# Performance work log

Hardware: AMD Instinct MI355X
Metric: run time of the kernel (lower is better)

The kernel has to match this reference:

```python
import jax, jax.numpy as jnp
import numpy as np

# Config mirroring My_MLP(mlp_layers=2, isize=512, k=30, non_linearity='relu',
#                        mlp_act='relu', offset_list=[2048]*4)
SIZES = [2048, 2048, 2048, 2048]   # per-client subgraph sizes (offset_list)
N = sum(SIZES)                      # 8192 total nodes
D = 512                             # isize
K = 30 + 1                          # module uses self.k + 1


def setup_inputs() -> dict:
    key = jax.random.key(0)
    k1, k2, k3 = jax.random.split(key, 3)
    features = jax.random.normal(k1, (N, D), dtype=jnp.float32)
    # Diag layer weights: a learned diagonal (vector) per layer, init near 1.
    w0 = 1.0 + 0.1 * jax.random.normal(k2, (D,), dtype=jnp.float32)
    w1 = 1.0 + 0.1 * jax.random.normal(k3, (D,), dtype=jnp.float32)
    return {"features": features, "w0": w0, "w1": w1}


def reference(features, w0, w1):
    # internal_forward: Diag -> relu -> Diag (no act after last layer)
    h = jax.nn.relu(features * w0) * w1                 # [N, D]
    # F.normalize(dim=1, p=2)
    emb = h * jax.lax.rsqrt(jnp.sum(h * h, axis=1, keepdims=True) + 1e-24)
    sim = jnp.matmul(emb, emb.T)                        # [N, N]

    # cross_subgraph_topk: per row, keep top-(k+1) similarities among columns
    # belonging to a DIFFERENT client subgraph; zero everything else.
    seg = jnp.asarray(np.repeat(np.arange(len(SIZES)), SIZES))   # [N] int
    same = seg[:, None] == seg[None, :]                           # [N, N] bool
    masked = jnp.where(same, -jnp.inf, sim)
    vals, inds = jax.lax.top_k(masked, K)                         # [N, K]
    rows = jnp.arange(N)[:, None]
    out = jnp.zeros_like(sim).at[rows, inds].set(vals)

    # apply_non_linearity('relu', i)
    return jax.nn.relu(out)
```

## Files before the change

kernel.cpp:

```cpp
#include <hip/hip_runtime.h>
#include <hip/hip_bf16.h>
#include <hip/hip_fp16.h>
#include <math.h>

typedef unsigned short u16;
typedef unsigned int u32;
typedef unsigned long long u64;
typedef __attribute__((ext_vector_type(8))) short bf16x8;
typedef __attribute__((ext_vector_type(4))) float f32x4;

#define N_NODES 8192
#define DIM 512
#define KSEL 31
#define BANDCAP 128
#define SEG_SIZE 2048
#define NVALID 6144
#define BAND_ULP 8

__device__ __forceinline__ u32 f16key(u32 h) {
  return (h & 0x8000u) ? (0xFFFFu & ~h) : (h | 0x8000u);
}
__device__ __forceinline__ u32 packkeys(u32 w) {
  return f16key(w & 0xFFFFu) | (f16key(w >> 16) << 16);
}
__device__ __forceinline__ float keyval(u32 k) {
  const u16 raw = (k & 0x8000u) ? (u16)(k ^ 0x8000u) : (u16)(~k & 0xFFFFu);
  __half_raw hr; hr.x = raw;
  return __half2float(__half(hr));
}

#define GLD_LDS16(g, l)                                        \
  __builtin_amdgcn_global_load_lds(                            \
      (const __attribute__((address_space(1))) void*)(g),      \
      (__attribute__((address_space(3))) void*)(l), 16, 0, 0)

__global__ __launch_bounds__(256) void prep_kernel(
    const float* __restrict__ feat, const float* __restrict__ w0,
    const float* __restrict__ w1, u16* __restrict__ embh,
    float* __restrict__ embf, u32* __restrict__ kmax32) {
#pragma clang fp contract(off)
  const int row = blockIdx.x;
  const int t = threadIdx.x;
  __shared__ float hs[DIM];
  __shared__ float partial[32];
  __shared__ float rinv_sh;

  const float2 x = *reinterpret_cast<const float2*>(feat + (size_t)row * DIM + t * 2);
  const float2 a = *reinterpret_cast<const float2*>(w0 + t * 2);
  const float2 b = *reinterpret_cast<const float2*>(w1 + t * 2);
  const float h0 = fmaxf(x.x * a.x, 0.0f) * b.x;
  const float h1 = fmaxf(x.y * a.y, 0.0f) * b.y;
  hs[t * 2] = h0;
  hs[t * 2 + 1] = h1;
  if (t == 0) kmax32[row] = 0u;
  __syncthreads();

  if (t < 32) {
    const int base = (t >> 3) * 128 + (t & 7);
    float v = hs[base];
    float acc = v * v;
    for (int i = 1; i < 16; ++i) {
      v = hs[base + 8 * i];
      const float vv = v * v;
      acc = acc + vv;
    }
    partial[t] = acc;
  }
  __syncthreads();
  if (t == 0) {
    float B[4];
    for (int blk = 0; blk < 4; ++blk) {
      const float* p = &partial[blk * 8];
      B[blk] = ((p[0] + p[1]) + (p[2] + p[3])) + ((p[4] + p[5]) + (p[6] + p[7]));
    }
    const float s = (B[0] + B[1]) + (B[2] + B[3]);
    const float sp = s + 1e-24f;
    const float qf = (float)sqrt((double)sp);
    rinv_sh = (float)(1.0 / (double)qf);
  }
  __syncthreads();
  const float rinv = rinv_sh;
  const float e0 = h0 * rinv;
  const float e1 = h1 * rinv;
  *reinterpret_cast<float2*>(embf + (size_t)row * DIM + t * 2) = make_float2(e0, e1);
  __hip_bfloat162 bb;
  bb.x = __float2bfloat16(e0);
  bb.y = __float2bfloat16(e1);
  *reinterpret_cast<__hip_bfloat162*>(embh + (size_t)row * DIM + t * 2) = bb;
}

__global__ __launch_bounds__(256) void gemm_kernel(const u16* __restrict__ embh,
                                                   __half* __restrict__ simh,
                                                   u32* __restrict__ kmax32) {
  const int tid = threadIdx.x;
  const int lane = tid & 63;
  const int wave = tid >> 6;
  const int wm = wave >> 1;
  const int wn = wave & 1;
  const int rowTile = blockIdx.y;
  const int segTileBase = (rowTile >> 4) << 4;
  const int cT = blockIdx.x;
  const int colTile = cT < segTileBase ? cT : cT + 16;
  if (colTile <= rowTile) return;
  const int row0 = rowTile * 128;
  const int col0 = colTile * 128;

  __shared__ u16 As[128][64];
  __shared__ u16 Bs[128][64];
  f32x4 acc[4][4] = {};

  for (int k0 = 0; k0 < DIM; k0 += 64) {
#pragma unroll
    for (int i = 0; i < 4; ++i) {
      const int flat = i * 256 + tid;
      const int r = flat >> 3;
      const int c = (flat & 7) * 8;
      GLD_LDS16(embh + (size_t)(row0 + r) * DIM + k0 + c, &As[r][c]);
      GLD_LDS16(embh + (size_t)(col0 + r) * DIM + k0 + c, &Bs[r][c]);
    }
    __syncthreads();
#pragma unroll
    for (int kk = 0; kk < 2; ++kk) {
      bf16x8 afr[4], bfr[4];
      const int koff = kk * 32 + (lane >> 4) * 8;
      const int rsel = lane & 15;
#pragma unroll
      for (int m = 0; m < 4; ++m)
        afr[m] = *reinterpret_cast<const bf16x8*>(&As[wm * 64 + m * 16 + rsel][koff]);
#pragma unroll
      for (int n = 0; n < 4; ++n)
        bfr[n] = *reinterpret_cast<const bf16x8*>(&Bs[wn * 64 + n * 16 + rsel][koff]);
#pragma unroll
      for (int m = 0; m < 4; ++m)
#pragma unroll
        for (int n = 0; n < 4; ++n)
          acc[m][n] = __builtin_amdgcn_mfma_f32_16x16x32_bf16(afr[m], bfr[n],
                                                              acc[m][n], 0, 0, 0);
    }
    __syncthreads();
  }

#pragma unroll
  for (int m = 0; m < 4; ++m)
#pragma unroll
    for (int n = 0; n < 4; ++n)
#pragma unroll
      for (int j = 0; j < 4; ++j) {
        const int r = row0 + wm * 64 + m * 16 + (lane >> 4) * 4 + j;
        const int pcol = cT * 128 + wn * 64 + n * 16 + (lane & 15);
        simh[(size_t)r * NVALID + pcol] = __float2half(acc[m][n][j]);
      }
  {
    const int segBaseC = (col0 >> 11) << 11;
    const int radj = (row0 < segBaseC) ? 0 : -SEG_SIZE;
#pragma unroll
    for (int m = 0; m < 4; ++m)
#pragma unroll
      for (int n = 0; n < 4; ++n) {
        const int c = col0 + wn * 64 + n * 16 + (lane & 15);
        const int rbase = row0 + wm * 64 + m * 16 + (lane >> 4) * 4;
        const __half h0 = __float2half(acc[m][n][0]);
        const __half h1 = __float2half(acc[m][n][1]);
        const __half h2 = __float2half(acc[m][n][2]);
        const __half h3 = __float2half(acc[m][n][3]);
        uint2 pkd;
        pkd.x = (u32)__half_as_ushort(h0) | ((u32)__half_as_ushort(h1) << 16);
        pkd.y = (u32)__half_as_ushort(h2) | ((u32)__half_as_ushort(h3) << 16);
        *reinterpret_cast<uint2*>(&simh[(size_t)c * NVALID + radj + rbase]) = pkd;
      }
  }
#pragma unroll
  for (int m = 0; m < 4; ++m) {
#pragma unroll
    for (int j = 0; j < 4; ++j) {
      float vmax = fmaxf(fmaxf(acc[m][0][j], acc[m][1][j]),
                         fmaxf(acc[m][2][j], acc[m][3][j]));
#pragma unroll
      for (int off = 1; off < 16; off <<= 1)
        vmax = fmaxf(vmax, __shfl_xor(vmax, off, 64));
      if ((lane & 15) == 0) {
        const int r = row0 + wm * 64 + m * 16 + (lane >> 4) * 4 + j;
        const u32 b = __float_as_uint(vmax);
        const u32 kk = (b & 0x80000000u) ? ~b : (b | 0x80000000u);
        atomicMax(&kmax32[r], kk);
      }
    }
  }
#pragma unroll
  for (int n = 0; n < 4; ++n) {
    float cmax = acc[0][n][0];
#pragma unroll
    for (int m = 0; m < 4; ++m)
#pragma unroll
      for (int j = 0; j < 4; ++j) cmax = fmaxf(cmax, acc[m][n][j]);
    cmax = fmaxf(cmax, __shfl_xor(cmax, 16, 64));
    cmax = fmaxf(cmax, __shfl_xor(cmax, 32, 64));
    if ((lane >> 4) == 0) {
      const int c = col0 + wn * 64 + n * 16 + (lane & 15);
      const u32 b = __float_as_uint(cmax);
      const u32 kk = (b & 0x80000000u) ? ~b : (b | 0x80000000u);
      atomicMax(&kmax32[c], kk);
    }
  }
}

__global__ __launch_bounds__(256) void select_kernel(
    const __half* __restrict__ simh, const float* __restrict__ embf,
    const u32* __restrict__ kmax32, int2* __restrict__ compact) {
  const int row = blockIdx.x;
  const int t = threadIdx.x;
  const int lane = t & 63;
  const int wave = t >> 6;

  __shared__ u32 hist[257];
  __shared__ int bcol[BANDCAP];
  __shared__ u32 bkey[BANDCAP];
  __shared__ float bex[BANDCAP];
  __shared__ int outidx_s[KSEL];
  __shared__ float outval_s[KSEL];
  __shared__ int cnts[2];
  __shared__ u32 sh_lo, sh_hi, sh_need;
  __shared__ int sh_state;

  const int segBase = (row >> 11) << 11;

  u32 pk[12];
  {
    const uint4* src = reinterpret_cast<const uint4*>(simh + (size_t)row * NVALID);
    const uint4 a = src[t], b = src[256 + t], c = src[512 + t];
    pk[0] = packkeys(a.x); pk[1] = packkeys(a.y);
    pk[2] = packkeys(a.z); pk[3] = packkeys(a.w);
    pk[4] = packkeys(b.x); pk[5] = packkeys(b.y);
    pk[6] = packkeys(b.z); pk[7] = packkeys(b.w);
    pk[8] = packkeys(c.x); pk[9] = packkeys(c.y);
    pk[10] = packkeys(c.z); pk[11] = packkeys(c.w);
  }
#define KEY(v) ((pk[(v) >> 1] >> (((v) & 1) * 16)) & 0xFFFFu)
#define COL(v) ((((((v) >> 3) * 256) + t) << 3) + ((v) & 7))

  if (t < KSEL) { outidx_s[t] = segBase; outval_s[t] = 0.0f; }
  if (t == 0) { cnts[0] = 0; cnts[1] = 0; }

  u32 kmax16;
  {
    const u32 kk = kmax32[row];
    const u32 fb = (kk & 0x80000000u) ? (kk ^ 0x80000000u) : ~kk;
    const __half h = __float2half(__uint_as_float(fb));
    kmax16 = f16key((u32)__half_as_ushort(h));
  }

  u32 base = (kmax16 > 4095u) ? kmax16 - 4095u : 0u;
  u32 winTop = kmax16;
  u32 shift = 4;
  u32 need = KSEL;
  for (int guard = 0; guard < 4; ++guard) {
    hist[t] = 0;
    if (t == 0) hist[256] = 0;
    __syncthreads();
#pragma unroll
    for (int v = 0; v < 24; ++v) {
      const u32 k = KEY(v);
      if (k >= base && k <= winTop) atomicAdd(&hist[(k - base) >> shift], 1u);
    }
    __syncthreads();
    if (wave == 0) {
      const int x = lane * 4;
      const u32 b0 = hist[x], b1 = hist[x + 1];
      const u32 b2 = hist[x + 2], b3 = hist[x + 3];
      const u32 tot = b0 + b1 + b2 + b3;
      u32 inc = tot;
#pragma unroll
      for (int off = 1; off < 64; off <<= 1) {
        const u32 vv = (u32)__shfl_down((int)inc, off, 64);
        if (lane + off < 64) inc += vv;
      }
      const u32 exc = inc - tot;
      const u32 g3 = exc, g2 = g3 + b3, g1 = g2 + b2, g0 = g1 + b1;
      int sel = -1;
      u32 gsel = 0;
      if (g3 < need && g3 + b3 >= need) { sel = x + 3; gsel = g3; }
      else if (g2 < need && g2 + b2 >= need) { sel = x + 2; gsel = g2; }
      else if (g1 < need && g1 + b1 >= need) { sel = x + 1; gsel = g1; }
      else if (g0 < need && g0 + b0 >= need) { sel = x;     gsel = g0; }
      const u64 bal = __ballot(sel >= 0);
      if (lane == 0 && bal == 0) sh_state = 0;
      if (bal != 0) {
        const int srcl = (int)(__ffsll((unsigned long long)bal) - 1);
        sel  = __shfl(sel, srcl, 64);
        gsel = (u32)__shfl((int)gsel, srcl, 64);
        if (lane == 0) {
          const u32 blo = base + ((u32)sel << shift);
          const u32 bhi = min(blo + (1u << shift) - 1u, winTop);
          sh_lo = blo; sh_hi = bhi; sh_need = need - gsel;
          sh_state = (shift > 4) ? 1 : 2;
        }
      }
    }
    __syncthreads();
    const int st = sh_state;
    if (st == 2) break;
    if (st == 1) {
      base = sh_lo; winTop = sh_hi; shift = 4; need = sh_need;
    } else {
      base = 0u; winTop = kmax16; shift = 8; need = KSEL;
    }
    __syncthreads();
  }
  const u32 binlo = sh_lo, binhi = sh_hi;
  const u32 hiK = binhi + BAND_ULP;
  const u32 loK = (binlo >= BAND_ULP) ? binlo - BAND_ULP : 0u;

#pragma unroll
  for (int v = 0; v < 24; ++v) {
    const u32 k = KEY(v);
    if (k > hiK) {
      const int slot = atomicAdd(&cnts[1], 1);
      const int i = COL(v);
      if (slot < KSEL) {
        outidx_s[slot] = (i < segBase) ? i : i + SEG_SIZE;
        outval_s[slot] = fmaxf(keyval(k), 0.0f);
      }
    } else if (k >= loK) {
      const int slot = atomicAdd(&cnts[0], 1);
      const int i = COL(v);
      if (slot < BANDCAP) {
        bcol[slot] = (i < segBase) ? i : i + SEG_SIZE;
        bkey[slot] = k;
      }
    }
  }
  __syncthreads();
  const int nH = min(cnts[1], KSEL);
  const int slots = KSEL - nH;
  const int nB = min(cnts[0], BANDCAP);

  if (nB == slots) {
    if (t < nB) {
      const int slot = atomicAdd(&cnts[1], 1);
      if (slot < KSEL) {
        outidx_s[slot] = bcol[t];
        outval_s[slot] = fmaxf(keyval(bkey[t]), 0.0f);
      }
    }
  } else {
    if (t < nB) {
#pragma clang fp contract(off)
      const float4* g4 =
          reinterpret_cast<const float4*>(embf + (size_t)bcol[t] * DIM);
      const float4* e4 = reinterpret_cast<const float4*>(embf + (size_t)row * DIM);
      float acc = 0.0f;
      for (int k4 = 0; k4 < DIM / 4; ++k4) {
        const float4 a = e4[k4];
        const float4 b = g4[k4];
        acc = acc + a.x * b.x;
        acc = acc + a.y * b.y;
        acc = acc + a.z * b.z;
        acc = acc + a.w * b.w;
      }
      bex[t] = acc;
    }
    __syncthreads();
    if (t < nB) {
      const float ev = bex[t];
      const int ec = bcol[t];
      int r = 0;
      for (int j = 0; j < nB; ++j) {
        const float oj = bex[j];
        const int cj = bcol[j];
        if (oj > ev || (oj == ev && cj < ec)) r++;
      }
      if (r < slots) {
        const int slot = atomicAdd(&cnts[1], 1);
        if (slot < KSEL) { outidx_s[slot] = ec; outval_s[slot] = fmaxf(ev, 0.0f); }
      }
    }
  }
  __syncthreads();
  if (t < KSEL)
    compact[(size_t)row * KSEL + t] =
        make_int2(outidx_s[t], __float_as_int(outval_s[t]));
#undef KEY
#undef COL
}

__global__ __launch_bounds__(256) void write_kernel(
    const int2* __restrict__ compact, float* __restrict__ out) {
  const int row = blockIdx.x;
  const int t = threadIdx.x;
  __shared__ int sidx[KSEL];
  __shared__ float sval[KSEL];
  if (t < KSEL) {
    const int2 e = compact[(size_t)row * KSEL + t];
    sidx[t] = e.x;
    sval[t] = __int_as_float(e.y);
  }
  float* orow = out + (size_t)row * N_NODES;
  const float4 zero4 = make_float4(0.f, 0.f, 0.f, 0.f);
  __syncthreads();
#pragma unroll
  for (int i = 0; i < 8; ++i)
    reinterpret_cast<float4*>(orow)[i * 256 + t] = zero4;
  __syncthreads();
  if (t < KSEL) orow[sidx[t]] = sval[t];
}

extern "C" void kernel_launch(void* const* d_in, const int* in_sizes, int n_in,
                              void* d_out, int out_size, void* d_ws, size_t ws_size,
                              hipStream_t stream) {
  const float* feat = (const float*)d_in[0];
  const float* w0 = (const float*)d_in[1];
  const float* w1 = (const float*)d_in[2];
  float* out = (float*)d_out;

  u16* embh = (u16*)d_ws;
  float* embf = (float*)((char*)d_ws + (size_t)N_NODES * DIM * 2);
  u32* kmax32 = (u32*)((char*)d_ws + (size_t)24 * 1024 * 1024);
  int2* compact = (int2*)d_ws;
  __half* simh = (__half*)d_out;

  prep_kernel<<<N_NODES, 256, 0, stream>>>(feat, w0, w1, embh, embf, kmax32);
  dim3 grid(48, 64);
  gemm_kernel<<<grid, 256, 0, stream>>>(embh, simh, kmax32);
  select_kernel<<<N_NODES, 256, 0, stream>>>(simh, embf, kmax32, compact);
  write_kernel<<<N_NODES, 256, 0, stream>>>(compact, out);
}
```

Measured before the change: 225.9 us.

## Prune top-k selection with per-32-column chunk maxima from GEMM epilogue

The GEMM epilogue now writes a per-row, per-32-column chunk maximum (as an f16 key) in place of global atomicMax row maxima. The select kernel uses these chunk maxima to build a coarse histogram, picks a threshold, and only reads and histograms the sim values in surviving chunks, so it no longer loads the full 6144-element row. The combined zero+write kernel is also split into a grid-stride zero kernel plus a separate scatter kernel. This cuts select-stage memory traffic and atomics, at the cost of more complex control flow, irregular gathered loads, and an extra launch.

After: 258.1 us. 1.14x slower.

```diff
diff --git a/kernel.cpp b/kernel.cpp
--- a/kernel.cpp
+++ b/kernel.cpp
@@ -15,19 +15,21 @@
 #define BANDCAP 128
 #define SEG_SIZE 2048
 #define NVALID 6144
+#define NCHUNK 192
 #define BAND_ULP 8
 
 __device__ __forceinline__ u32 f16key(u32 h) {
   return (h & 0x8000u) ? (0xFFFFu & ~h) : (h | 0x8000u);
-}
-__device__ __forceinline__ u32 packkeys(u32 w) {
-  return f16key(w & 0xFFFFu) | (f16key(w >> 16) << 16);
 }
 __device__ __forceinline__ float keyval(u32 k) {
   const u16 raw = (k & 0x8000u) ? (u16)(k ^ 0x8000u) : (u16)(~k & 0xFFFFu);
   __half_raw hr; hr.x = raw;
   return __half2float(__half(hr));
 }
+__device__ __forceinline__ u16 key16(float v) {
+  const __half h = __float2half(v);
+  return (u16)f16key((u32)__half_as_ushort(h));
+}
 
 #define GLD_LDS16(g, l)                                        \
   __builtin_amdgcn_global_load_lds(                            \
@@ -37,7 +39,7 @@
 __global__ __launch_bounds__(256) void prep_kernel(
     const float* __restrict__ feat, const float* __restrict__ w0,
     const float* __restrict__ w1, u16* __restrict__ embh,
-    float* __restrict__ embf, u32* __restrict__ kmax32) {
+    float* __restrict__ embf) {
 #pragma clang fp contract(off)
   const int row = blockIdx.x;
   const int t = threadIdx.x;
@@ -52,7 +54,6 @@
   const float h1 = fmaxf(x.y * a.y, 0.0f) * b.y;
   hs[t * 2] = h0;
   hs[t * 2 + 1] = h1;
-  if (t == 0) kmax32[row] = 0u;
   __syncthreads();
 
   if (t < 32) {
@@ -91,7 +92,7 @@
 
 __global__ __launch_bounds__(256) void gemm_kernel(const u16* __restrict__ embh,
                                                    __half* __restrict__ simh,
-                                                   u32* __restrict__ kmax32) {
+                                                   u16* __restrict__ cmax) {
   const int tid = threadIdx.x;
   const int lane = tid & 63;
   const int wave = tid >> 6;
@@ -150,116 +151,160 @@
         const int pcol = cT * 128 + wn * 64 + n * 16 + (lane & 15);
         simh[(size_t)r * NVALID + pcol] = __float2half(acc[m][n][j]);
       }
-  {
-    const int segBaseC = (col0 >> 11) << 11;
-    const int radj = (row0 < segBaseC) ? 0 : -SEG_SIZE;
-#pragma unroll
-    for (int m = 0; m < 4; ++m)
-#pragma unroll
-      for (int n = 0; n < 4; ++n) {
+  const int segBaseC = (col0 >> 11) << 11;
+  const int radj = (row0 < segBaseC) ? 0 : -SEG_SIZE;
+#pragma unroll
+  for (int m = 0; m < 4; ++m)
+#pragma unroll
+    for (int n = 0; n < 4; ++n) {
+      const int c = col0 + wn * 64 + n * 16 + (lane & 15);
+      const int rbase = row0 + wm * 64 + m * 16 + (lane >> 4) * 4;
+      const __half h0 = __float2half(acc[m][n][0]);
+      const __half h1 = __float2half(acc[m][n][1]);
+      const __half h2 = __float2half(acc[m][n][2]);
+      const __half h3 = __float2half(acc[m][n][3]);
+      uint2 pkd;
+      pkd.x = (u32)__half_as_ushort(h0) | ((u32)__half_as_ushort(h1) << 16);
+      pkd.y = (u32)__half_as_ushort(h2) | ((u32)__half_as_ushort(h3) << 16);
+      *reinterpret_cast<uint2*>(&simh[(size_t)c * NVALID + radj + rbase]) = pkd;
+    }
+
+#pragma unroll
+  for (int m = 0; m < 4; ++m)
+#pragma unroll
+    for (int j = 0; j < 4; ++j)
+#pragma unroll
+      for (int p = 0; p < 2; ++p) {
+        float v = fmaxf(acc[m][2 * p][j], acc[m][2 * p + 1][j]);
+#pragma unroll
+        for (int off = 1; off < 16; off <<= 1)
+          v = fmaxf(v, __shfl_xor(v, off, 64));
+        if ((lane & 15) == 0) {
+          const int r = row0 + wm * 64 + m * 16 + (lane >> 4) * 4 + j;
+          cmax[(size_t)r * NCHUNK + cT * 4 + wn * 2 + p] = key16(v);
+        }
+      }
+#pragma unroll
+  for (int n = 0; n < 4; ++n)
+#pragma unroll
+    for (int q = 0; q < 2; ++q) {
+      float v = acc[2 * q][n][0];
+#pragma unroll
+      for (int j = 1; j < 4; ++j) v = fmaxf(v, acc[2 * q][n][j]);
+#pragma unroll
+      for (int j = 0; j < 4; ++j) v = fmaxf(v, acc[2 * q + 1][n][j]);
+      v = fmaxf(v, __shfl_xor(v, 16, 64));
+      v = fmaxf(v, __shfl_xor(v, 32, 64));
+      if ((lane >> 4) == 0) {
         const int c = col0 + wn * 64 + n * 16 + (lane & 15);
-        const int rbase = row0 + wm * 64 + m * 16 + (lane >> 4) * 4;
-        const __half h0 = __float2half(acc[m][n][0]);
-        const __half h1 = __float2half(acc[m][n][1]);
-        const __half h2 = __float2half(acc[m][n][2]);
-        const __half h3 = __float2half(acc[m][n][3]);
-        uint2 pkd;
-        pkd.x = (u32)__half_as_ushort(h0) | ((u32)__half_as_ushort(h1) << 16);
-        pkd.y = (u32)__half_as_ushort(h2) | ((u32)__half_as_ushort(h3) << 16);
-        *reinterpret_cast<uint2*>(&simh[(size_t)c * NVALID + radj + rbase]) = pkd;
-      }
-  }
-#pragma unroll
-  for (int m = 0; m < 4; ++m) {
-#pragma unroll
-    for (int j = 0; j < 4; ++j) {
-      float vmax = fmaxf(fmaxf(acc[m][0][j], acc[m][1][j]),
-                         fmaxf(acc[m][2][j], acc[m][3][j]));
-#pragma unroll
-      for (int off = 1; off < 16; off <<= 1)
-        vmax = fmaxf(vmax, __shfl_xor(vmax, off, 64));
-      if ((lane & 15) == 0) {
-        const int r = row0 + wm * 64 + m * 16 + (lane >> 4) * 4 + j;
-        const u32 b = __float_as_uint(vmax);
-        const u32 kk = (b & 0x80000000u) ? ~b : (b | 0x80000000u);
-        atomicMax(&kmax32[r], kk);
-      }
-    }
-  }
-#pragma unroll
-  for (int n = 0; n < 4; ++n) {
-    float cmax = acc[0][n][0];
-#pragma unroll
-    for (int m = 0; m < 4; ++m)
-#pragma unroll
-      for (int j = 0; j < 4; ++j) cmax = fmaxf(cmax, acc[m][n][j]);
-    cmax = fmaxf(cmax, __shfl_xor(cmax, 16, 64));
-    cmax = fmaxf(cmax, __shfl_xor(cmax, 32, 64));
-    if ((lane >> 4) == 0) {
-      const int c = col0 + wn * 64 + n * 16 + (lane & 15);
-      const u32 b = __float_as_uint(cmax);
-      const u32 kk = (b & 0x80000000u) ? ~b : (b | 0x80000000u);
-      atomicMax(&kmax32[c], kk);
-    }
-  }
+        cmax[(size_t)c * NCHUNK + ((radj + row0) >> 5) + wm * 2 + q] = key16(v);
+      }
+    }
 }
 
 __global__ __launch_bounds__(256) void select_kernel(
     const __half* __restrict__ simh, const float* __restrict__ embf,
-    const u32* __restrict__ kmax32, int2* __restrict__ compact) {
+    const u16* __restrict__ cmax, int2* __restrict__ compact) {
   const int row = blockIdx.x;
   const int t = threadIdx.x;
   const int lane = t & 63;
   const int wave = t >> 6;
 
+  __shared__ __align__(16) u16 cmk[NCHUNK];
+  __shared__ u16 survc[NCHUNK];
   __shared__ u32 hist[257];
   __shared__ int bcol[BANDCAP];
   __shared__ u32 bkey[BANDCAP];
   __shared__ float bex[BANDCAP];
   __shared__ int outidx_s[KSEL];
   __shared__ float outval_s[KSEL];
-  __shared__ int cnts[2];
+  __shared__ int cnts[3];
   __shared__ u32 sh_lo, sh_hi, sh_need;
   __shared__ int sh_state;
+  __shared__ u32 kmax_sh, T_sh;
+  __shared__ u32 wred[4];
 
   const int segBase = (row >> 11) << 11;
-
-  u32 pk[12];
+  const u16* srow = reinterpret_cast<const u16*>(simh + (size_t)row * NVALID);
+
+  if (t < 24)
+    reinterpret_cast<uint4*>(cmk)[t] =
+        reinterpret_cast<const uint4*>(cmax + (size_t)row * NCHUNK)[t];
+  hist[t] = 0;
+  if (t == 0) { hist[256] = 0; cnts[0] = 0; cnts[1] = 0; cnts[2] = 0; }
+  if (t < KSEL) { outidx_s[t] = segBase; outval_s[t] = 0.0f; }
+  __syncthreads();
+
   {
-    const uint4* src = reinterpret_cast<const uint4*>(simh + (size_t)row * NVALID);
-    const uint4 a = src[t], b = src[256 + t], c = src[512 + t];
-    pk[0] = packkeys(a.x); pk[1] = packkeys(a.y);
-    pk[2] = packkeys(a.z); pk[3] = packkeys(a.w);
-    pk[4] = packkeys(b.x); pk[5] = packkeys(b.y);
-    pk[6] = packkeys(b.z); pk[7] = packkeys(b.w);
-    pk[8] = packkeys(c.x); pk[9] = packkeys(c.y);
-    pk[10] = packkeys(c.z); pk[11] = packkeys(c.w);
-  }
-#define KEY(v) ((pk[(v) >> 1] >> (((v) & 1) * 16)) & 0xFFFFu)
-#define COL(v) ((((((v) >> 3) * 256) + t) << 3) + ((v) & 7))
-
-  if (t < KSEL) { outidx_s[t] = segBase; outval_s[t] = 0.0f; }
-  if (t == 0) { cnts[0] = 0; cnts[1] = 0; }
-
-  u32 kmax16;
-  {
-    const u32 kk = kmax32[row];
-    const u32 fb = (kk & 0x80000000u) ? (kk ^ 0x80000000u) : ~kk;
-    const __half h = __float2half(__uint_as_float(fb));
-    kmax16 = f16key((u32)__half_as_ushort(h));
-  }
+    u32 m = (t < NCHUNK) ? (u32)cmk[t] : 0u;
+#pragma unroll
+    for (int off = 1; off < 64; off <<= 1)
+      m = max(m, (u32)__shfl_xor((int)m, off, 64));
+    if (lane == 0) wred[wave] = m;
+    __syncthreads();
+    if (t == 0)
+      kmax_sh = max(max(wred[0], wred[1]), max(wred[2], wred[3]));
+    __syncthreads();
+  }
+  const u32 kmax16 = kmax_sh;
+  const u32 baseA = (kmax16 > 4095u) ? kmax16 - 4095u : 0u;
+
+  if (t < NCHUNK) {
+    const u32 k = cmk[t];
+    if (k >= baseA) atomicAdd(&hist[(k - baseA) >> 4], 1u);
+  }
+  __syncthreads();
+  if (wave == 0) {
+    const int x = lane * 4;
+    const u32 b0 = hist[x], b1 = hist[x + 1];
+    const u32 b2 = hist[x + 2], b3 = hist[x + 3];
+    const u32 tot = b0 + b1 + b2 + b3;
+    u32 inc = tot;
+#pragma unroll
+    for (int off = 1; off < 64; off <<= 1) {
+      const u32 vv = (u32)__shfl_down((int)inc, off, 64);
+      if (lane + off < 64) inc += vv;
+    }
+    const u32 exc = inc - tot;
+    const u32 need = KSEL;
+    const u32 g3 = exc, g2 = g3 + b3, g1 = g2 + b2, g0 = g1 + b1;
+    int sel = -1;
+    if (g3 < need && g3 + b3 >= need) sel = x + 3;
+    else if (g2 < need && g2 + b2 >= need) sel = x + 2;
+    else if (g1 < need && g1 + b1 >= need) sel = x + 1;
+    else if (g0 < need && g0 + b0 >= need) sel = x;
+    const u64 bal = __ballot(sel >= 0);
+    if (bal == 0) {
+      if (lane == 0) T_sh = 0u;
+    } else {
+      const int srcl = (int)(__ffsll((unsigned long long)bal) - 1);
+      sel = __shfl(sel, srcl, 64);
+      if (lane == 0) {
+        const u32 blo = baseA + ((u32)sel << 4);
+        T_sh = (blo >= 32u) ? blo - 32u : 0u;
+      }
+    }
+  }
+  __syncthreads();
+  const u32 T = T_sh;
+
+  if (t < NCHUNK && (u32)cmk[t] >= T) {
+    const int s = atomicAdd(&cnts[2], 1);
+    survc[s] = (u16)t;
+  }
+  hist[t] = 0;
+  if (t == 0) hist[256] = 0;
+  __syncthreads();
+  int nSurv = cnts[2];
 
   u32 base = (kmax16 > 4095u) ? kmax16 - 4095u : 0u;
   u32 winTop = kmax16;
   u32 shift = 4;
   u32 need = KSEL;
   for (int guard = 0; guard < 4; ++guard) {
-    hist[t] = 0;
-    if (t == 0) hist[256] = 0;
-    __syncthreads();
-#pragma unroll
-    for (int v = 0; v < 24; ++v) {
-      const u32 k = KEY(v);
+    for (int i = t; i < nSurv * 32; i += 256) {
+      const int ch = survc[i >> 5];
+      const u32 k = f16key((u32)srow[(ch << 5) | (i & 31)]);
       if (k >= base && k <= winTop) atomicAdd(&hist[(k - base) >> shift], 1u);
     }
     __syncthreads();
@@ -302,29 +347,32 @@
     if (st == 1) {
       base = sh_lo; winTop = sh_hi; shift = 4; need = sh_need;
     } else {
+      if (t < NCHUNK) survc[t] = (u16)t;
+      nSurv = NCHUNK;
       base = 0u; winTop = kmax16; shift = 8; need = KSEL;
     }
+    hist[t] = 0;
+    if (t == 0) hist[256] = 0;
     __syncthreads();
   }
   const u32 binlo = sh_lo, binhi = sh_hi;
   const u32 hiK = binhi + BAND_ULP;
   const u32 loK = (binlo >= BAND_ULP) ? binlo - BAND_ULP : 0u;
 
-#pragma unroll
-  for (int v = 0; v < 24; ++v) {
-    const u32 k = KEY(v);
+  for (int i = t; i < nSurv * 32; i += 256) {
+    const int ch = survc[i >> 5];
+    const int pcol = (ch << 5) | (i & 31);
+    const u32 k = f16key((u32)srow[pcol]);
     if (k > hiK) {
       const int slot = atomicAdd(&cnts[1], 1);
-      const int i = COL(v);
       if (slot < KSEL) {
-        outidx_s[slot] = (i < segBase) ? i : i + SEG_SIZE;
+        outidx_s[slot] = (pcol < segBase) ? pcol : pcol + SEG_SIZE;
         outval_s[slot] = fmaxf(keyval(k), 0.0f);
       }
     } else if (k >= loK) {
       const int slot = atomicAdd(&cnts[0], 1);
-      const int i = COL(v);
       if (slot < BANDCAP) {
-        bcol[slot] = (i < segBase) ? i : i + SEG_SIZE;
+        bcol[slot] = (pcol < segBase) ? pcol : pcol + SEG_SIZE;
         bkey[slot] = k;
       }
     }
@@ -379,29 +427,23 @@
   if (t < KSEL)
     compact[(size_t)row * KSEL + t] =
         make_int2(outidx_s[t], __float_as_int(outval_s[t]));
-#undef KEY
-#undef COL
-}
-
-__global__ __launch_bounds__(256) void write_kernel(
+}
+
+__global__ __launch_bounds__(256) void zero_kernel(float4* __restrict__ out4) {
+  const size_t total = (size_t)N_NODES * N_NODES / 4;
+  const float4 z = make_float4(0.f, 0.f, 0.f, 0.f);
+  for (size_t i = (size_t)blockIdx.x * 256 + threadIdx.x; i < total;
+       i += (size_t)gridDim.x * 256)
+    out4[i] = z;
+}
+
+__global__ __launch_bounds__(256) void scatter_kernel(
     const int2* __restrict__ compact, float* __restrict__ out) {
-  const int row = blockIdx.x;
-  const int t = threadIdx.x;
-  __shared__ int sidx[KSEL];
-  __shared__ float sval[KSEL];
-  if (t < KSEL) {
-    const int2 e = compact[(size_t)row * KSEL + t];
-    sidx[t] = e.x;
-    sval[t] = __int_as_float(e.y);
-  }
-  float* orow = out + (size_t)row * N_NODES;
-  const float4 zero4 = make_float4(0.f, 0.f, 0.f, 0.f);
-  __syncthreads();
-#pragma unroll
-  for (int i = 0; i < 8; ++i)
-    reinterpret_cast<float4*>(orow)[i * 256 + t] = zero4;
-  __syncthreads();
-  if (t < KSEL) orow[sidx[t]] = sval[t];
+  const int gid = blockIdx.x * 256 + threadIdx.x;
+  if (gid >= N_NODES * KSEL) return;
+  const int row = gid / KSEL;
+  const int2 e = compact[gid];
+  out[(size_t)row * N_NODES + e.x] = __int_as_float(e.y);
 }
 
 extern "C" void kernel_launch(void* const* d_in, const int* in_sizes, int n_in,
@@ -414,13 +456,14 @@
 
   u16* embh = (u16*)d_ws;
   float* embf = (float*)((char*)d_ws + (size_t)N_NODES * DIM * 2);
-  u32* kmax32 = (u32*)((char*)d_ws + (size_t)24 * 1024 * 1024);
+  u16* cmax = (u16*)((char*)d_ws + (size_t)24 * 1024 * 1024);
   int2* compact = (int2*)d_ws;
   __half* simh = (__half*)d_out;
 
-  prep_kernel<<<N_NODES, 256, 0, stream>>>(feat, w0, w1, embh, embf, kmax32);
+  prep_kernel<<<N_NODES, 256, 0, stream>>>(feat, w0, w1, embh, embf);
   dim3 grid(48, 64);
-  gemm_kernel<<<grid, 256, 0, stream>>>(embh, simh, kmax32);
-  select_kernel<<<N_NODES, 256, 0, stream>>>(simh, embf, kmax32, compact);
-  write_kernel<<<N_NODES, 256, 0, stream>>>(compact, out);
-}
+  gemm_kernel<<<grid, 256, 0, stream>>>(embh, simh, cmax);
+  select_kernel<<<N_NODES, 256, 0, stream>>>(simh, embf, cmax, compact);
+  zero_kernel<<<4096, 256, 0, stream>>>((float4*)out);
+  scatter_kernel<<<(N_NODES * KSEL + 255) / 256, 256, 0, stream>>>(compact, out);
+}
```
